# Kernel optimization log

Hardware: AMD Instinct MI355X
Metric: run time of the kernel (lower is better)

The kernel has to match this reference:

```python
import jax, jax.numpy as jnp
import numpy as np

ROUTE = 64            # route_size (square)
NLEV = 4              # resolution_num = [0,1,2,3]
LOSS_W = (1.0, 1.0, 1.0, 1.0)


def _sumpool(x, k):
    # non-overlapping sum pool, kernel=stride=k; x: (B,1,H,W) with H,W divisible by k
    B, C, H, W = x.shape
    return x.reshape(B, C, H // k, k, W // k, k).sum(axis=(3, 5))


def _up_nearest(x, k):
    # nearest upsample by integer factor k on the two trailing dims
    return jnp.repeat(jnp.repeat(x, k, axis=2), k, axis=3)


def _unfold(x, k):
    # F.unfold(x, k, stride=k) then .transpose(2,1).view(B,L,k,k) for C==1
    B, C, H, W = x.shape
    ph, pw = H // k, W // k
    return x.reshape(B, ph, k, pw, k).transpose(0, 1, 3, 2, 4).reshape(B, ph * pw, k, k)


def _fold(p, H, W, k):
    # inverse of _unfold: p (B, L, k, k) -> (B,1,H,W)
    B, L, _, _ = p.shape
    ph, pw = H // k, W // k
    return p.reshape(B, ph, pw, k, k).transpose(0, 1, 3, 2, 4).reshape(B, 1, H, W)


def setup_inputs() -> dict:
    key = jax.random.key(0)
    ks = jax.random.split(key, 8)
    B, H = 8, 1024
    d = {}
    for i in range(NLEV):
        s = (B, 1, H >> i, H >> i)
        d[f'out{i}'] = jax.random.uniform(ks[i], s, dtype=jnp.float32)
        d[f'gt{i}'] = jax.random.uniform(ks[4 + i], s, dtype=jnp.float32)
    return d


def reference(out0, out1, out2, out3, gt0, gt1, gt2, gt3):
    out_list = [out0, out1, out2, out3]
    label_list = [gt0, gt1, gt2, gt3]
    B, _, H, W = out0.shape

    # ---- get_moe_label: per-patch routing score on detached maps ----
    scores = []
    for i in range(NLEV):
        k = ROUTE >> i
        pre = jax.lax.stop_gradient(out_list[i])
        gt = jax.lax.stop_gradient(label_list[i])
        err = (pre - gt) ** 2
        patch_err = _sumpool(err, k)                      # (B,1,ph,pw)
        patch_mse = patch_err / (k * k)
        fractions = _sumpool(gt, k)
        scores.append(patch_mse + patch_err / (fractions + 1e-10))
    score = jnp.concatenate(scores, axis=1)               # (B,4,ph,pw)
    moe_label = jnp.argmin(score, axis=1, keepdims=True)  # (B,1,ph,pw) int

    # mask_gt = scatter one-hot of moe_label along channel dim
    mask_gt = (moe_label == jnp.arange(NLEV, dtype=moe_label.dtype)[None, :, None, None]).astype(score.dtype)

    mask_add = jnp.ones_like(mask_gt[:, :1])              # (B,1,ph,pw)
    loss = jnp.zeros((), dtype=out0.dtype)
    label_patch = None
    moe_flat = moe_label.reshape(B, -1)                   # (B, L)

    for i in range(NLEV):
        k = ROUTE >> i
        loss_mask = _up_nearest(mask_add, k)              # matches out_list[i] spatial size
        hard = jnp.mean((out_list[i] * loss_mask - label_list[i] * loss_mask) ** 2)
        loss = loss + hard * LOSS_W[i]
        if i == 0:
            lp = label_list[0] * _up_nearest(mask_gt[:, 0:1], ROUTE)
            label_patch = _unfold(lp, ROUTE)              # (B, L, 64, 64)
        else:
            gsl = _unfold(label_list[i], k)               # (B, L, k, k)
            pad = (ROUTE - k) // 2
            gsl = jnp.pad(gsl, ((0, 0), (0, 0), (pad, pad), (pad, pad)), constant_values=0.2)
            pick = (moe_flat == i)[:, :, None, None]
            label_patch = label_patch + gsl * pick
        mask_add = mask_add - mask_gt[:, i:i + 1]

    label_patch = _fold(label_patch, H, W, ROUTE)         # (B,1,H,W)
    return loss[None], label_patch, moe_label, score
```

## Files before the change

kernel.cpp:

```cpp
#include <hip/hip_runtime.h>


#define NPATCH 2048

__global__ __launch_bounds__(256) void fused_score_kernel(
    const float* __restrict__ out0, const float* __restrict__ gt0,
    const float* __restrict__ out1, const float* __restrict__ gt1,
    const float* __restrict__ out2, const float* __restrict__ gt2,
    const float* __restrict__ out3, const float* __restrict__ gt3,
    float* __restrict__ scoreOut,
    float* __restrict__ moeF,
    int* __restrict__ moeI,
    double* __restrict__ lossTerm)
{
    const int p = blockIdx.x;
    const int b = p >> 8;
    const int l = p & 255;
    const int py = l >> 4, px = l & 15;

    const float* PO[4] = {out0, out1, out2, out3};
    const float* PG[4] = {gt0, gt1, gt2, gt3};

    float err[4], gts[4];

    #pragma unroll
    for (int lev = 0; lev < 4; ++lev) {
        const int k  = 64 >> lev;
        const int W  = 1024 >> lev;
        const int kv = k >> 2;
        const int nvec = k * kv;
        const int rowBase = py * k, colBase = px * k;
        const size_t base = (size_t)b * W * W;
        const float* po = PO[lev];
        const float* pg = PG[lev];

        float e = 0.f, g = 0.f;
        for (int idx = threadIdx.x; idx < nvec; idx += 256) {
            int r = idx / kv;
            int c = (idx % kv) * 4;
            size_t off = base + (size_t)(rowBase + r) * W + (colBase + c);
            float4 o = *(const float4*)(po + off);
            float4 q = *(const float4*)(pg + off);
            float dx = o.x - q.x, dy = o.y - q.y, dz = o.z - q.z, dw = o.w - q.w;
            e += dx * dx + dy * dy + dz * dz + dw * dw;
            g += q.x + q.y + q.z + q.w;
        }
        err[lev] = e; gts[lev] = g;
    }

    for (int s = 32; s; s >>= 1) {
        #pragma unroll
        for (int i = 0; i < 4; ++i) {
            err[i] += __shfl_down(err[i], s, 64);
            gts[i] += __shfl_down(gts[i], s, 64);
        }
    }
    __shared__ float se[4][4], sg[4][4];
    const int wave = threadIdx.x >> 6, lane = threadIdx.x & 63;
    if (lane == 0) {
        #pragma unroll
        for (int i = 0; i < 4; ++i) { se[i][wave] = err[i]; sg[i][wave] = gts[i]; }
    }
    __syncthreads();
    if (threadIdx.x == 0) {
        float E[4], S[4];
        #pragma unroll
        for (int i = 0; i < 4; ++i) {
            E[i] = se[i][0] + se[i][1] + se[i][2] + se[i][3];
            float G = sg[i][0] + sg[i][1] + sg[i][2] + sg[i][3];
            float kk = (float)((64 >> i) * (64 >> i));
            S[i] = E[i] / kk + E[i] / (G + 1e-10f);
            scoreOut[b * 1024 + i * 256 + l] = S[i];
        }
        int m = 0; float best = S[0];
        #pragma unroll
        for (int i = 1; i < 4; ++i)
            if (S[i] < best) { best = S[i]; m = i; }
        moeF[p] = (float)m;
        moeI[p] = m;
        double t = (double)E[0] / 8388608.0;
        if (m >= 1) t += (double)E[1] / 2097152.0;
        if (m >= 2) t += (double)E[2] / 524288.0;
        if (m >= 3) t += (double)E[3] / 131072.0;
        lossTerm[p] = t;
    }
}

__global__ __launch_bounds__(256) void label_loss_kernel(
    const float* __restrict__ gt0, const float* __restrict__ gt1,
    const float* __restrict__ gt2, const float* __restrict__ gt3,
    const int* __restrict__ moe, const double* __restrict__ lossTerm,
    float* __restrict__ lossOut, float* __restrict__ lab)
{
    if (blockIdx.x == 0) {
        double t = 0.0;
        for (int i = threadIdx.x; i < NPATCH; i += 256) t += lossTerm[i];
        for (int s = 32; s; s >>= 1) t += __shfl_down(t, s, 64);
        __shared__ double sd[4];
        const int wave = threadIdx.x >> 6, lane = threadIdx.x & 63;
        if (lane == 0) sd[wave] = t;
        __syncthreads();
        if (threadIdx.x == 0)
            lossOut[0] = (float)(sd[0] + sd[1] + sd[2] + sd[3]);
    }

    int g = blockIdx.x * 256 + threadIdx.x;
    int b = g >> 20;
    int rem = g & 1048575;
    int y = rem >> 10, x = rem & 1023;
    int py = y >> 6, px = x >> 6;
    int m = moe[(b << 8) + (py << 4) + px];
    float v;
    if (m == 0) {
        v = gt0[g];
    } else {
        int k = 64 >> m, pad = (64 - k) >> 1, W = 1024 >> m;
        int iy = (y & 63) - pad;
        int ix = (x & 63) - pad;
        if ((unsigned)iy < (unsigned)k && (unsigned)ix < (unsigned)k) {
            const float* gt = (m == 1) ? gt1 : (m == 2) ? gt2 : gt3;
            v = gt[b * W * W + (py * k + iy) * W + (px * k + ix)];
        } else {
            v = 0.2f;
        }
    }
    lab[g] = v;
}

extern "C" void kernel_launch(void* const* d_in, const int* in_sizes, int n_in,
                              void* d_out, int out_size, void* d_ws, size_t ws_size,
                              hipStream_t stream) {
    const float* out0 = (const float*)d_in[0];
    const float* gt0  = (const float*)d_in[1];
    const float* out1 = (const float*)d_in[2];
    const float* gt1  = (const float*)d_in[3];
    const float* out2 = (const float*)d_in[4];
    const float* gt2  = (const float*)d_in[5];
    const float* out3 = (const float*)d_in[6];
    const float* gt3  = (const float*)d_in[7];

    float* o = (float*)d_out;
    float* lossOut  = o;
    float* labOut   = o + 1;
    float* moeFOut  = o + 8388609;
    float* scoreOut = o + 8390657;

    double* lossTerm = (double*)d_ws;
    int*    moeI     = (int*)((char*)d_ws + 16384);

    fused_score_kernel<<<NPATCH, 256, 0, stream>>>(
        out0, gt0, out1, gt1, out2, gt2, out3, gt3,
        scoreOut, moeFOut, moeI, lossTerm);
    label_loss_kernel<<<32768, 256, 0, stream>>>(
        gt0, gt1, gt2, gt3, moeI, lossTerm, lossOut, labOut);
}
```

Measured before the change: 38.01 us.

## Fuse label-patch write into score kernel with atomic ticket loss reduction

Merges the label-assembly kernel into the per-patch score kernel, so each block writes its own 64x64 label patch as soon as it has the routing decision. gt0 was just read by the same block and may still be cached. The loss is now accumulated through a fixed-point 64-bit atomic add, and a last-block ticket writes the final value. This removes one kernel launch and the moe/lossTerm round trip through memory. In exchange it adds a memset launch, scalar (non-vectorised) label copies, and the fixed-point scaling could overflow or lose precision.

```diff
diff --git a/kernel.cpp b/kernel.cpp
--- a/kernel.cpp
+++ b/kernel.cpp
@@ -2,16 +2,19 @@
 
 
 #define NPATCH 2048
+#define LOSS_SCALE 18014398509481984.0
 
-__global__ __launch_bounds__(256) void fused_score_kernel(
+__global__ __launch_bounds__(256) void fused_kernel(
     const float* __restrict__ out0, const float* __restrict__ gt0,
     const float* __restrict__ out1, const float* __restrict__ gt1,
     const float* __restrict__ out2, const float* __restrict__ gt2,
     const float* __restrict__ out3, const float* __restrict__ gt3,
     float* __restrict__ scoreOut,
     float* __restrict__ moeF,
-    int* __restrict__ moeI,
-    double* __restrict__ lossTerm)
+    float* __restrict__ lab,
+    float* __restrict__ lossOut,
+    unsigned long long* __restrict__ lossAcc,
+    unsigned int* __restrict__ ticket)
 {
     const int p = blockIdx.x;
     const int b = p >> 8;
@@ -56,6 +59,7 @@
         }
     }
     __shared__ float se[4][4], sg[4][4];
+    __shared__ int sm;
     const int wave = threadIdx.x >> 6, lane = threadIdx.x & 63;
     if (lane == 0) {
         #pragma unroll
@@ -77,54 +81,44 @@
         for (int i = 1; i < 4; ++i)
             if (S[i] < best) { best = S[i]; m = i; }
         moeF[p] = (float)m;
-        moeI[p] = m;
+        sm = m;
         double t = (double)E[0] / 8388608.0;
         if (m >= 1) t += (double)E[1] / 2097152.0;
         if (m >= 2) t += (double)E[2] / 524288.0;
         if (m >= 3) t += (double)E[3] / 131072.0;
-        lossTerm[p] = t;
-    }
-}
-
-__global__ __launch_bounds__(256) void label_loss_kernel(
-    const float* __restrict__ gt0, const float* __restrict__ gt1,
-    const float* __restrict__ gt2, const float* __restrict__ gt3,
-    const int* __restrict__ moe, const double* __restrict__ lossTerm,
-    float* __restrict__ lossOut, float* __restrict__ lab)
-{
-    if (blockIdx.x == 0) {
-        double t = 0.0;
-        for (int i = threadIdx.x; i < NPATCH; i += 256) t += lossTerm[i];
-        for (int s = 32; s; s >>= 1) t += __shfl_down(t, s, 64);
-        __shared__ double sd[4];
-        const int wave = threadIdx.x >> 6, lane = threadIdx.x & 63;
-        if (lane == 0) sd[wave] = t;
-        __syncthreads();
-        if (threadIdx.x == 0)
-            lossOut[0] = (float)(sd[0] + sd[1] + sd[2] + sd[3]);
-    }
-
-    int g = blockIdx.x * 256 + threadIdx.x;
-    int b = g >> 20;
-    int rem = g & 1048575;
-    int y = rem >> 10, x = rem & 1023;
-    int py = y >> 6, px = x >> 6;
-    int m = moe[(b << 8) + (py << 4) + px];
-    float v;
-    if (m == 0) {
-        v = gt0[g];
-    } else {
-        int k = 64 >> m, pad = (64 - k) >> 1, W = 1024 >> m;
-        int iy = (y & 63) - pad;
-        int ix = (x & 63) - pad;
-        if ((unsigned)iy < (unsigned)k && (unsigned)ix < (unsigned)k) {
-            const float* gt = (m == 1) ? gt1 : (m == 2) ? gt2 : gt3;
-            v = gt[b * W * W + (py * k + iy) * W + (px * k + ix)];
-        } else {
-            v = 0.2f;
+        unsigned long long fx = (unsigned long long)llrint(t * LOSS_SCALE);
+        atomicAdd(lossAcc, fx);
+        __threadfence();
+        unsigned int tk = atomicAdd(ticket, 1u);
+        if (tk == NPATCH - 1) {
+            unsigned long long total = atomicAdd(lossAcc, 0ULL);
+            lossOut[0] = (float)((double)total / LOSS_SCALE);
         }
     }
-    lab[g] = v;
+    __syncthreads();
+    const int m = sm;
+
+    const size_t labBase = (size_t)b * 1048576 + (size_t)(py * 64) * 1024 + px * 64;
+    if (m == 0) {
+        for (int idx = threadIdx.x; idx < 4096; idx += 256) {
+            int y = idx >> 6, x = idx & 63;
+            size_t off = labBase + (size_t)y * 1024 + x;
+            size_t goff = (size_t)b * 1048576 + (size_t)(py * 64 + y) * 1024 + (px * 64 + x);
+            lab[off] = gt0[goff];
+        }
+    } else {
+        const int k = 64 >> m, pad = (64 - k) >> 1, W = 1024 >> m;
+        const float* gt = (m == 1) ? gt1 : (m == 2) ? gt2 : gt3;
+        const size_t gbase = (size_t)b * W * W;
+        for (int idx = threadIdx.x; idx < 4096; idx += 256) {
+            int y = idx >> 6, x = idx & 63;
+            int iy = y - pad, ix = x - pad;
+            float v = 0.2f;
+            if ((unsigned)iy < (unsigned)k && (unsigned)ix < (unsigned)k)
+                v = gt[gbase + (size_t)(py * k + iy) * W + (px * k + ix)];
+            lab[labBase + (size_t)y * 1024 + x] = v;
+        }
+    }
 }
 
 extern "C" void kernel_launch(void* const* d_in, const int* in_sizes, int n_in,
@@ -145,12 +139,12 @@
     float* moeFOut  = o + 8388609;
     float* scoreOut = o + 8390657;
 
-    double* lossTerm = (double*)d_ws;
-    int*    moeI     = (int*)((char*)d_ws + 16384);
+    unsigned long long* lossAcc = (unsigned long long*)d_ws;
+    unsigned int* ticket = (unsigned int*)((char*)d_ws + 8);
 
-    fused_score_kernel<<<NPATCH, 256, 0, stream>>>(
+    hipMemsetAsync(d_ws, 0, 16, stream);
+
+    fused_kernel<<<NPATCH, 256, 0, stream>>>(
         out0, gt0, out1, gt1, out2, gt2, out3, gt3,
-        scoreOut, moeFOut, moeI, lossTerm);
-    label_loss_kernel<<<32768, 256, 0, stream>>>(
-        gt0, gt1, gt2, gt3, moeI, lossTerm, lossOut, labOut);
+        scoreOut, moeFOut, labOut, lossOut, lossAcc, ticket);
 }
```

Result: slower. 91.51 us (+140.7%).

## Fuse label-patch writing into per-patch score kernel

Applied to the files above, without the earlier changes.

Each score block now writes its own 64x64 label patch right after choosing the routing level, instead of a second 32768-block kernel re-reading the moe index and gathering per pixel. The loss reduction moves to a tiny single-block kernel. Because the label output sits at offset 1, the code writes three head elements and one tail element per row as scalars and the rest as aligned float4 stores. This cuts a big launch and the moe round trip, and gt0 for level 0 is likely still in cache. The trade-off is a block-level sync and fewer blocks doing the label writes.

```diff
diff --git a/kernel.cpp b/kernel.cpp
--- a/kernel.cpp
+++ b/kernel.cpp
@@ -3,14 +3,14 @@
 
 #define NPATCH 2048
 
-__global__ __launch_bounds__(256) void fused_score_kernel(
+__global__ __launch_bounds__(256) void fused_kernel(
     const float* __restrict__ out0, const float* __restrict__ gt0,
     const float* __restrict__ out1, const float* __restrict__ gt1,
     const float* __restrict__ out2, const float* __restrict__ gt2,
     const float* __restrict__ out3, const float* __restrict__ gt3,
     float* __restrict__ scoreOut,
     float* __restrict__ moeF,
-    int* __restrict__ moeI,
+    float* __restrict__ lab,
     double* __restrict__ lossTerm)
 {
     const int p = blockIdx.x;
@@ -56,6 +56,7 @@
         }
     }
     __shared__ float se[4][4], sg[4][4];
+    __shared__ int sm;
     const int wave = threadIdx.x >> 6, lane = threadIdx.x & 63;
     if (lane == 0) {
         #pragma unroll
@@ -77,54 +78,87 @@
         for (int i = 1; i < 4; ++i)
             if (S[i] < best) { best = S[i]; m = i; }
         moeF[p] = (float)m;
-        moeI[p] = m;
+        sm = m;
         double t = (double)E[0] / 8388608.0;
         if (m >= 1) t += (double)E[1] / 2097152.0;
         if (m >= 2) t += (double)E[2] / 524288.0;
         if (m >= 3) t += (double)E[3] / 131072.0;
         lossTerm[p] = t;
     }
+    __syncthreads();
+    const int m = sm;
+
+    const size_t labBase = (size_t)b * 1048576 + (size_t)(py * 64) * 1024 + px * 64;
+
+    if (m == 0) {
+        for (int idx = threadIdx.x; idx < 1024; idx += 256) {
+            int y = idx >> 4, j = idx & 15;
+            size_t R0 = labBase + (size_t)y * 1024;
+            if (j < 15) {
+                int x = 3 + 4 * j;
+                float4 v;
+                v.x = gt0[R0 + x];
+                v.y = gt0[R0 + x + 1];
+                v.z = gt0[R0 + x + 2];
+                v.w = gt0[R0 + x + 3];
+                *(float4*)(lab + R0 + x) = v;
+            } else {
+                lab[R0]     = gt0[R0];
+                lab[R0 + 1] = gt0[R0 + 1];
+                lab[R0 + 2] = gt0[R0 + 2];
+                lab[R0 + 63] = gt0[R0 + 63];
+            }
+        }
+    } else {
+        const int k = 64 >> m, pad = (64 - k) >> 1, W = 1024 >> m;
+        const float* gt = (m == 1) ? gt1 : (m == 2) ? gt2 : gt3;
+        const size_t gbase = (size_t)b * W * W + (size_t)(py * k) * W + px * k;
+        for (int idx = threadIdx.x; idx < 1024; idx += 256) {
+            int y = idx >> 4, j = idx & 15;
+            size_t R0 = labBase + (size_t)y * 1024;
+            int iy = y - pad;
+            bool rowIn = (unsigned)iy < (unsigned)k;
+            const float* grow = gt + gbase + (size_t)iy * W;
+            if (j < 15) {
+                int x = 3 + 4 * j;
+                float4 v;
+                #pragma unroll
+                for (int u = 0; u < 4; ++u) {
+                    int ix = x + u - pad;
+                    float vv = 0.2f;
+                    if (rowIn && (unsigned)ix < (unsigned)k) vv = grow[ix];
+                    ((float*)&v)[u] = vv;
+                }
+                *(float4*)(lab + R0 + x) = v;
+            } else {
+                #pragma unroll
+                for (int u = 0; u < 3; ++u) {
+                    int ix = u - pad;
+                    float vv = 0.2f;
+                    if (rowIn && (unsigned)ix < (unsigned)k) vv = grow[ix];
+                    lab[R0 + u] = vv;
+                }
+                int ix = 63 - pad;
+                float vv = 0.2f;
+                if (rowIn && (unsigned)ix < (unsigned)k) vv = grow[ix];
+                lab[R0 + 63] = vv;
+            }
+        }
+    }
 }
 
-__global__ __launch_bounds__(256) void label_loss_kernel(
-    const float* __restrict__ gt0, const float* __restrict__ gt1,
-    const float* __restrict__ gt2, const float* __restrict__ gt3,
-    const int* __restrict__ moe, const double* __restrict__ lossTerm,
-    float* __restrict__ lossOut, float* __restrict__ lab)
+__global__ __launch_bounds__(256) void loss_kernel(
+    const double* __restrict__ lossTerm, float* __restrict__ lossOut)
 {
-    if (blockIdx.x == 0) {
-        double t = 0.0;
-        for (int i = threadIdx.x; i < NPATCH; i += 256) t += lossTerm[i];
-        for (int s = 32; s; s >>= 1) t += __shfl_down(t, s, 64);
-        __shared__ double sd[4];
-        const int wave = threadIdx.x >> 6, lane = threadIdx.x & 63;
-        if (lane == 0) sd[wave] = t;
-        __syncthreads();
-        if (threadIdx.x == 0)
-            lossOut[0] = (float)(sd[0] + sd[1] + sd[2] + sd[3]);
-    }
-
-    int g = blockIdx.x * 256 + threadIdx.x;
-    int b = g >> 20;
-    int rem = g & 1048575;
-    int y = rem >> 10, x = rem & 1023;
-    int py = y >> 6, px = x >> 6;
-    int m = moe[(b << 8) + (py << 4) + px];
-    float v;
-    if (m == 0) {
-        v = gt0[g];
-    } else {
-        int k = 64 >> m, pad = (64 - k) >> 1, W = 1024 >> m;
-        int iy = (y & 63) - pad;
-        int ix = (x & 63) - pad;
-        if ((unsigned)iy < (unsigned)k && (unsigned)ix < (unsigned)k) {
-            const float* gt = (m == 1) ? gt1 : (m == 2) ? gt2 : gt3;
-            v = gt[b * W * W + (py * k + iy) * W + (px * k + ix)];
-        } else {
-            v = 0.2f;
-        }
-    }
-    lab[g] = v;
+    double t = 0.0;
+    for (int i = threadIdx.x; i < NPATCH; i += 256) t += lossTerm[i];
+    for (int s = 32; s; s >>= 1) t += __shfl_down(t, s, 64);
+    __shared__ double sd[4];
+    const int wave = threadIdx.x >> 6, lane = threadIdx.x & 63;
+    if (lane == 0) sd[wave] = t;
+    __syncthreads();
+    if (threadIdx.x == 0)
+        lossOut[0] = (float)(sd[0] + sd[1] + sd[2] + sd[3]);
 }
 
 extern "C" void kernel_launch(void* const* d_in, const int* in_sizes, int n_in,
@@ -146,11 +180,9 @@
     float* scoreOut = o + 8390657;
 
     double* lossTerm = (double*)d_ws;
-    int*    moeI     = (int*)((char*)d_ws + 16384);
 
-    fused_score_kernel<<<NPATCH, 256, 0, stream>>>(
+    fused_kernel<<<NPATCH, 256, 0, stream>>>(
         out0, gt0, out1, gt1, out2, gt2, out3, gt3,
-        scoreOut, moeFOut, moeI, lossTerm);
-    label_loss_kernel<<<32768, 256, 0, stream>>>(
-        gt0, gt1, gt2, gt3, moeI, lossTerm, lossOut, labOut);
+        scoreOut, moeFOut, labOut, lossTerm);
+    loss_kernel<<<1, 256, 0, stream>>>(lossTerm, lossOut);
 }
```

After: 30.83 us. -18.9%, faster.
